# Performance work log

Hardware: AMD Instinct MI355X
Metric: run time of the kernel (lower is better)

The kernel has to match this reference:

```python
import jax, jax.numpy as jnp
import numpy as np


def setup_inputs() -> dict:
    key = jax.random.key(0)
    k1, k2, k3 = jax.random.split(key, 3)
    B, C, H, W = 4, 16, 64, 64
    F, K = 32, 3
    x = jax.random.normal(k1, (B, C, H, W), dtype=jnp.float32)
    # Pade coefficients per (out_channel, in_channel, a, b): numerator deg 5, denom deg 4.
    nums = jax.random.normal(k2, (F, C, K, K, 6), dtype=jnp.float32) * 0.3
    denoms = jax.random.normal(k3, (F, C, K, K, 4), dtype=jnp.float32) * 0.3
    return {"x": x, "nums": nums, "denoms": denoms}


def _rational_conv(x, nums, denoms):
    B, C, H, W = x.shape
    F, _, K, _, _ = nums.shape
    p = (K - 1) // 2
    # pad spatially, move channels last: (B, H+2p, W+2p, C)
    xp = jnp.pad(x, ((0, 0), (0, 0), (p, p), (p, p))).transpose(0, 2, 3, 1)
    # im2col patches: stack the K*K shifted views -> (B, H, W, K2, C)
    patches = jnp.stack(
        [xp[:, a:a + H, b:b + W, :] for a in range(K) for b in range(K)], axis=3
    )
    # powers x^0..x^5 built by repeated multiply (safe for negative bases)
    pws = [jnp.ones_like(patches)]
    for _ in range(5):
        pws.append(pws[-1] * patches)
    pw = jnp.stack(pws, axis=-1)                         # (B,H,W,K2,C,6)
    nums_r = nums.reshape(F, C, K * K, 6)                # (a,b) flattened a*K+b, matches patch order
    denoms_r = denoms.reshape(F, C, K * K, 4)
    # P(x) = sum_n a_n x^n ; Q(x) = 1 + |sum_m b_m x^m|, m=1..4  (Pade version A)
    P = jnp.einsum('bhwkcn,fckn->bhwfkc', pw, nums_r)
    Q = 1.0 + jnp.abs(jnp.einsum('bhwkcm,fckm->bhwfkc', pw[..., 1:5], denoms_r))
    out = (P / Q).sum(axis=(4, 5))                       # (B,H,W,F)
    return out.transpose(0, 3, 1, 2)                     # (B,F,H,W)


def reference(x, nums, denoms):
    return _rational_conv(x, nums, denoms)
```

## Files before the change

### kernel.cpp

```cpp
#include <hip/hip_runtime.h>

#define B_ 4
#define C_ 16
#define H_ 64
#define W_ 64
#define F_ 32
#define R_ 16
#define NT_ (H_ / R_)

__global__ __launch_bounds__(256)
void ka_rconv_kernel(const float* __restrict__ xin,
                     const float* __restrict__ nums,
                     const float* __restrict__ denoms,
                     float* __restrict__ out) {
    const int tid = threadIdx.x;
    int bid = blockIdx.x;
    const int f    = bid & (F_ - 1);  bid >>= 5;
    const int tile = bid & (NT_ - 1);
    const int b    = bid >> 2;
    const int row0 = tile * R_;

    const int g   = tid & 15;
    const int r   = tid >> 4;
    const int w0  = g * 4;
    const int gy0 = row0 + r;

    float acc[4] = {0.f, 0.f, 0.f, 0.f};

    const float* nbase = nums   + f * (C_ * 54);
    const float* dbase = denoms + f * (C_ * 36);
    const float* xb    = xin + (size_t)b * C_ * H_ * W_ + w0;

    #pragma unroll 2
    for (int c = 0; c < C_; ++c) {
        const float* xc = xb + c * (H_ * W_);
        float row[3][6];
        #pragma unroll
        for (int a = 0; a < 3; ++a) {
            const int gy   = gy0 + a - 1;
            const bool rok = (gy >= 0) && (gy < H_);
            const float* rp = xc + gy * W_;
            float4 m = rok ? *(const float4*)rp : make_float4(0.f, 0.f, 0.f, 0.f);
            float lo = (rok && (w0 > 0))       ? rp[-1] : 0.f;
            float hi = (rok && (w0 + 4 < W_))  ? rp[4]  : 0.f;
            row[a][0] = lo;  row[a][1] = m.x; row[a][2] = m.y;
            row[a][3] = m.z; row[a][4] = m.w; row[a][5] = hi;
        }

        const float* np = nbase + c * 54;
        const float* dp = dbase + c * 36;
        #pragma unroll
        for (int a = 0; a < 3; ++a) {
            #pragma unroll
            for (int bb = 0; bb < 3; ++bb) {
                const int t = a * 3 + bb;
                const float n0 = np[t*6+0], n1 = np[t*6+1], n2 = np[t*6+2];
                const float n3 = np[t*6+3], n4 = np[t*6+4], n5 = np[t*6+5];
                const float d0 = dp[t*4+0], d1 = dp[t*4+1], d2 = dp[t*4+2], d3 = dp[t*4+3];
                #pragma unroll
                for (int p = 0; p < 4; ++p) {
                    const float xv = row[a][bb + p];
                    float P = fmaf(n5, xv, n4);
                    P = fmaf(P, xv, n3);
                    P = fmaf(P, xv, n2);
                    P = fmaf(P, xv, n1);
                    P = fmaf(P, xv, n0);
                    float Q = fmaf(d3, xv, d2);
                    Q = fmaf(Q, xv, d1);
                    Q = fmaf(Q, xv, d0);
                    Q *= xv;
                    Q = 1.0f + fabsf(Q);
                    acc[p] = fmaf(P, __builtin_amdgcn_rcpf(Q), acc[p]);
                }
            }
        }
    }

    float* op = out + (((size_t)b * F_ + f) * H_ + gy0) * W_ + w0;
    *(float4*)op = make_float4(acc[0], acc[1], acc[2], acc[3]);
}

extern "C" void kernel_launch(void* const* d_in, const int* in_sizes, int n_in,
                              void* d_out, int out_size, void* d_ws, size_t ws_size,
                              hipStream_t stream) {
    const float* x      = (const float*)d_in[0];
    const float* nums   = (const float*)d_in[1];
    const float* denoms = (const float*)d_in[2];
    float* outp = (float*)d_out;
    dim3 grid(B_ * NT_ * F_);
    ka_rconv_kernel<<<grid, 256, 0, stream>>>(x, nums, denoms, outp);
}
```

Before: 93.49 us.

## Map one output pixel per thread with 4-row tiles instead of 4-wide strips

Each thread now computes a single output pixel instead of four horizontally adjacent ones. Each block covers 4 rows by 64 columns, which gives four times as many blocks. Loads become nine scalar coalesced loads per channel using precomputed clamped offsets and validity masks, replacing float4 plus halo loads. This raises parallelism and occupancy and lowers register use. The cost is that each thread loses reuse of its coefficient loads across four pixels, and each block does redundant halo loads.

```diff
diff --git a/kernel.cpp b/kernel.cpp
--- a/kernel.cpp
+++ b/kernel.cpp
@@ -5,8 +5,6 @@
 #define H_ 64
 #define W_ 64
 #define F_ 32
-#define R_ 16
-#define NT_ (H_ / R_)
 
 __global__ __launch_bounds__(256)
 void ka_rconv_kernel(const float* __restrict__ xin,
@@ -14,38 +12,49 @@
                      const float* __restrict__ denoms,
                      float* __restrict__ out) {
     const int tid = threadIdx.x;
+    const int col = tid & 63;
+    const int r   = tid >> 6;
+
     int bid = blockIdx.x;
-    const int f    = bid & (F_ - 1);  bid >>= 5;
-    const int tile = bid & (NT_ - 1);
-    const int b    = bid >> 2;
-    const int row0 = tile * R_;
+    const int f = bid & (F_ - 1);  bid >>= 5;
+    const int q = bid & 15;        bid >>= 4;
+    const int b = bid;
+    const int gy = q * 4 + r;
 
-    const int g   = tid & 15;
-    const int r   = tid >> 4;
-    const int w0  = g * 4;
-    const int gy0 = row0 + r;
-
-    float acc[4] = {0.f, 0.f, 0.f, 0.f};
+    int   offs[3][3];
+    bool  ok[3][3];
+    #pragma unroll
+    for (int a = 0; a < 3; ++a) {
+        const int gy2 = gy + a - 1;
+        const bool vy = (gy2 >= 0) & (gy2 < H_);
+        const int gyc = min(max(gy2, 0), H_ - 1);
+        #pragma unroll
+        for (int bb = 0; bb < 3; ++bb) {
+            const int gx2 = col + bb - 1;
+            const bool vx = (gx2 >= 0) & (gx2 < W_);
+            const int gxc = min(max(gx2, 0), W_ - 1);
+            offs[a][bb] = gyc * W_ + gxc;
+            ok[a][bb]   = vy & vx;
+        }
+    }
 
     const float* nbase = nums   + f * (C_ * 54);
     const float* dbase = denoms + f * (C_ * 36);
-    const float* xb    = xin + (size_t)b * C_ * H_ * W_ + w0;
+    const float* xb    = xin + (size_t)b * C_ * H_ * W_;
+
+    float acc = 0.f;
 
     #pragma unroll 2
     for (int c = 0; c < C_; ++c) {
         const float* xc = xb + c * (H_ * W_);
-        float row[3][6];
+        float xv[3][3];
         #pragma unroll
-        for (int a = 0; a < 3; ++a) {
-            const int gy   = gy0 + a - 1;
-            const bool rok = (gy >= 0) && (gy < H_);
-            const float* rp = xc + gy * W_;
-            float4 m = rok ? *(const float4*)rp : make_float4(0.f, 0.f, 0.f, 0.f);
-            float lo = (rok && (w0 > 0))       ? rp[-1] : 0.f;
-            float hi = (rok && (w0 + 4 < W_))  ? rp[4]  : 0.f;
-            row[a][0] = lo;  row[a][1] = m.x; row[a][2] = m.y;
-            row[a][3] = m.z; row[a][4] = m.w; row[a][5] = hi;
-        }
+        for (int a = 0; a < 3; ++a)
+            #pragma unroll
+            for (int bb = 0; bb < 3; ++bb) {
+                float v = xc[offs[a][bb]];
+                xv[a][bb] = ok[a][bb] ? v : 0.f;
+            }
 
         const float* np = nbase + c * 54;
         const float* dp = dbase + c * 36;
@@ -54,30 +63,23 @@
             #pragma unroll
             for (int bb = 0; bb < 3; ++bb) {
                 const int t = a * 3 + bb;
-                const float n0 = np[t*6+0], n1 = np[t*6+1], n2 = np[t*6+2];
-                const float n3 = np[t*6+3], n4 = np[t*6+4], n5 = np[t*6+5];
-                const float d0 = dp[t*4+0], d1 = dp[t*4+1], d2 = dp[t*4+2], d3 = dp[t*4+3];
-                #pragma unroll
-                for (int p = 0; p < 4; ++p) {
-                    const float xv = row[a][bb + p];
-                    float P = fmaf(n5, xv, n4);
-                    P = fmaf(P, xv, n3);
-                    P = fmaf(P, xv, n2);
-                    P = fmaf(P, xv, n1);
-                    P = fmaf(P, xv, n0);
-                    float Q = fmaf(d3, xv, d2);
-                    Q = fmaf(Q, xv, d1);
-                    Q = fmaf(Q, xv, d0);
-                    Q *= xv;
-                    Q = 1.0f + fabsf(Q);
-                    acc[p] = fmaf(P, __builtin_amdgcn_rcpf(Q), acc[p]);
-                }
+                const float xvv = xv[a][bb];
+                float P = fmaf(np[t*6+5], xvv, np[t*6+4]);
+                P = fmaf(P, xvv, np[t*6+3]);
+                P = fmaf(P, xvv, np[t*6+2]);
+                P = fmaf(P, xvv, np[t*6+1]);
+                P = fmaf(P, xvv, np[t*6+0]);
+                float Q = fmaf(dp[t*4+3], xvv, dp[t*4+2]);
+                Q = fmaf(Q, xvv, dp[t*4+1]);
+                Q = fmaf(Q, xvv, dp[t*4+0]);
+                Q *= xvv;
+                Q = 1.0f + fabsf(Q);
+                acc = fmaf(P, __builtin_amdgcn_rcpf(Q), acc);
             }
         }
     }
 
-    float* op = out + (((size_t)b * F_ + f) * H_ + gy0) * W_ + w0;
-    *(float4*)op = make_float4(acc[0], acc[1], acc[2], acc[3]);
+    out[(((size_t)b * F_ + f) * H_ + gy) * W_ + col] = acc;
 }
 
 extern "C" void kernel_launch(void* const* d_in, const int* in_sizes, int n_in,
@@ -87,6 +89,6 @@
     const float* nums   = (const float*)d_in[1];
     const float* denoms = (const float*)d_in[2];
     float* outp = (float*)d_out;
-    dim3 grid(B_ * NT_ * F_);
+    dim3 grid(B_ * 16 * F_);
     ka_rconv_kernel<<<grid, 256, 0, stream>>>(x, nums, denoms, outp);
 }
```

Result: no change. 93.09 us (-0.4%).

## Remap threads to one column with two vertical outputs and double grid

Applied to the files above, without the earlier changes.

Each thread now computes one column and two vertically adjacent outputs instead of four horizontal outputs. Each block covers 8 rows instead of 16, which doubles the number of blocks. Neighbour loads become per-thread scalar gathers through precomputed clamped offsets and zero masks instead of float4 row loads. This spreads the work over more blocks and simplifies the boundary handling, at the cost of less per-thread instruction-level parallelism and less vectorised loading.

```diff
diff --git a/kernel.cpp b/kernel.cpp
--- a/kernel.cpp
+++ b/kernel.cpp
@@ -5,8 +5,6 @@
 #define H_ 64
 #define W_ 64
 #define F_ 32
-#define R_ 16
-#define NT_ (H_ / R_)
 
 __global__ __launch_bounds__(256)
 void ka_rconv_kernel(const float* __restrict__ xin,
@@ -14,70 +12,84 @@
                      const float* __restrict__ denoms,
                      float* __restrict__ out) {
     const int tid = threadIdx.x;
+    const int col = tid & 63;
+    const int rp  = tid >> 6;
+
     int bid = blockIdx.x;
-    const int f    = bid & (F_ - 1);  bid >>= 5;
-    const int tile = bid & (NT_ - 1);
-    const int b    = bid >> 2;
-    const int row0 = tile * R_;
+    const int f  = bid & 31;  bid >>= 5;
+    const int t8 = bid & 7;   bid >>= 3;
+    const int b  = bid;
+    const int gy0 = t8 * 8 + rp * 2;
 
-    const int g   = tid & 15;
-    const int r   = tid >> 4;
-    const int w0  = g * 4;
-    const int gy0 = row0 + r;
-
-    float acc[4] = {0.f, 0.f, 0.f, 0.f};
+    int   off[4][3];
+    float msk[4][3];
+    #pragma unroll
+    for (int a = 0; a < 4; ++a) {
+        const int gy   = gy0 + a - 1;
+        const bool vy  = (gy >= 0) && (gy < H_);
+        const int gyc  = min(max(gy, 0), H_ - 1);
+        #pragma unroll
+        for (int j = 0; j < 3; ++j) {
+            const int gx  = col + j - 1;
+            const bool vx = (gx >= 0) && (gx < W_);
+            const int gxc = min(max(gx, 0), W_ - 1);
+            off[a][j] = gyc * W_ + gxc;
+            msk[a][j] = (vy && vx) ? 1.0f : 0.0f;
+        }
+    }
 
     const float* nbase = nums   + f * (C_ * 54);
     const float* dbase = denoms + f * (C_ * 36);
-    const float* xb    = xin + (size_t)b * C_ * H_ * W_ + w0;
+    const float* xb    = xin + (size_t)b * C_ * (H_ * W_);
 
-    #pragma unroll 2
+    float acc0 = 0.f, acc1 = 0.f;
+
     for (int c = 0; c < C_; ++c) {
         const float* xc = xb + c * (H_ * W_);
-        float row[3][6];
+        float xv[4][3];
         #pragma unroll
-        for (int a = 0; a < 3; ++a) {
-            const int gy   = gy0 + a - 1;
-            const bool rok = (gy >= 0) && (gy < H_);
-            const float* rp = xc + gy * W_;
-            float4 m = rok ? *(const float4*)rp : make_float4(0.f, 0.f, 0.f, 0.f);
-            float lo = (rok && (w0 > 0))       ? rp[-1] : 0.f;
-            float hi = (rok && (w0 + 4 < W_))  ? rp[4]  : 0.f;
-            row[a][0] = lo;  row[a][1] = m.x; row[a][2] = m.y;
-            row[a][3] = m.z; row[a][4] = m.w; row[a][5] = hi;
-        }
+        for (int a = 0; a < 4; ++a)
+            #pragma unroll
+            for (int j = 0; j < 3; ++j)
+                xv[a][j] = xc[off[a][j]] * msk[a][j];
 
         const float* np = nbase + c * 54;
         const float* dp = dbase + c * 36;
         #pragma unroll
         for (int a = 0; a < 3; ++a) {
             #pragma unroll
-            for (int bb = 0; bb < 3; ++bb) {
-                const int t = a * 3 + bb;
+            for (int j = 0; j < 3; ++j) {
+                const int t = a * 3 + j;
                 const float n0 = np[t*6+0], n1 = np[t*6+1], n2 = np[t*6+2];
                 const float n3 = np[t*6+3], n4 = np[t*6+4], n5 = np[t*6+5];
                 const float d0 = dp[t*4+0], d1 = dp[t*4+1], d2 = dp[t*4+2], d3 = dp[t*4+3];
-                #pragma unroll
-                for (int p = 0; p < 4; ++p) {
-                    const float xv = row[a][bb + p];
-                    float P = fmaf(n5, xv, n4);
-                    P = fmaf(P, xv, n3);
-                    P = fmaf(P, xv, n2);
-                    P = fmaf(P, xv, n1);
-                    P = fmaf(P, xv, n0);
-                    float Q = fmaf(d3, xv, d2);
-                    Q = fmaf(Q, xv, d1);
-                    Q = fmaf(Q, xv, d0);
-                    Q *= xv;
-                    Q = 1.0f + fabsf(Q);
-                    acc[p] = fmaf(P, __builtin_amdgcn_rcpf(Q), acc[p]);
-                }
+
+                const float x0 = xv[a][j];
+                const float x1 = xv[a + 1][j];
+
+                float P0 = fmaf(n5, x0, n4);
+                float P1 = fmaf(n5, x1, n4);
+                P0 = fmaf(P0, x0, n3);  P1 = fmaf(P1, x1, n3);
+                P0 = fmaf(P0, x0, n2);  P1 = fmaf(P1, x1, n2);
+                P0 = fmaf(P0, x0, n1);  P1 = fmaf(P1, x1, n1);
+                P0 = fmaf(P0, x0, n0);  P1 = fmaf(P1, x1, n0);
+
+                float Q0 = fmaf(d3, x0, d2);
+                float Q1 = fmaf(d3, x1, d2);
+                Q0 = fmaf(Q0, x0, d1);  Q1 = fmaf(Q1, x1, d1);
+                Q0 = fmaf(Q0, x0, d0);  Q1 = fmaf(Q1, x1, d0);
+                Q0 *= x0;               Q1 *= x1;
+                Q0 = 1.0f + fabsf(Q0);  Q1 = 1.0f + fabsf(Q1);
+
+                acc0 = fmaf(P0, __builtin_amdgcn_rcpf(Q0), acc0);
+                acc1 = fmaf(P1, __builtin_amdgcn_rcpf(Q1), acc1);
             }
         }
     }
 
-    float* op = out + (((size_t)b * F_ + f) * H_ + gy0) * W_ + w0;
-    *(float4*)op = make_float4(acc[0], acc[1], acc[2], acc[3]);
+    float* op = out + (((size_t)b * F_ + f) * H_ + gy0) * W_ + col;
+    op[0]  = acc0;
+    op[W_] = acc1;
 }
 
 extern "C" void kernel_launch(void* const* d_in, const int* in_sizes, int n_in,
@@ -87,6 +99,6 @@
     const float* nums   = (const float*)d_in[1];
     const float* denoms = (const float*)d_in[2];
     float* outp = (float*)d_out;
-    dim3 grid(B_ * NT_ * F_);
+    dim3 grid(B_ * 8 * F_);
     ka_rconv_kernel<<<grid, 256, 0, stream>>>(x, nums, denoms, outp);
 }
```

Measured after the change: 87.80 us. -6.1%, faster.
